# Kernel tuning notes

Hardware: AMD Instinct MI355X
Metric: run time of the kernel (lower is better)

The kernel has to match this reference:

```python
import jax, jax.numpy as jnp
import numpy as np

B, L, D_IN, D_OUT, H = 2, 2048, 1024, 1024, 16
HD = D_OUT // H


def setup_inputs() -> dict:
    key = jax.random.key(0)
    ks = jax.random.split(key, 7)
    s_in = 1.0 / np.sqrt(D_IN)
    s_out = 1.0 / np.sqrt(D_OUT)
    return {
        "x": jax.random.normal(ks[0], (B, L, D_IN), dtype=jnp.float32),
        "Wq": jax.random.uniform(ks[1], (D_OUT, D_IN), jnp.float32, -s_in, s_in),
        "Wg": jax.random.uniform(ks[2], (D_OUT, D_IN), jnp.float32, -s_in, s_in),
        "Wk": jax.random.uniform(ks[3], (D_OUT, D_IN), jnp.float32, -s_in, s_in),
        "Wv": jax.random.uniform(ks[4], (D_OUT, D_IN), jnp.float32, -s_in, s_in),
        "Wo": jax.random.uniform(ks[5], (D_OUT, D_OUT), jnp.float32, -s_out, s_out),
        "bo": jax.random.uniform(ks[6], (D_OUT,), jnp.float32, -s_out, s_out),
    }


def reference(x, Wq, Wg, Wk, Wv, Wo, bo):
    b, l, _ = x.shape
    # projections (torch Linear: x @ W^T)
    q = jnp.einsum('bld,od->blo', x, Wq).reshape(b, l, H, HD)
    g = jnp.einsum('bld,od->blo', x, Wg)
    k = jnp.einsum('bld,od->blo', x, Wk).reshape(b, l, H, HD)
    v = jnp.einsum('bld,od->blo', x, Wv).reshape(b, l, H, HD)
    # attention scores [B,H,L,L]
    scores = jnp.einsum('bqhd,bkhd->bhqk', q, k)
    causal = jnp.tril(jnp.ones((l, l), dtype=bool))
    neg = jnp.finfo(scores.dtype).min
    scores = jnp.where(causal[None, None], scores, neg)
    attn = jax.nn.softmax(scores / np.sqrt(HD), axis=-1)
    ctx = jnp.einsum('bhqk,bkhd->bqhd', attn, v).reshape(b, l, D_OUT)
    ctx = ctx * jax.nn.sigmoid(g)
    return jnp.einsum('blo,po->blp', ctx, Wo) + bo
```

## Files before the change

kernel.cpp:

```cpp
#include <hip/hip_runtime.h>
#include <hip/hip_bf16.h>


typedef __bf16 v8bf __attribute__((ext_vector_type(8)));
typedef __bf16 v4bf __attribute__((ext_vector_type(4)));
typedef float  v4f  __attribute__((ext_vector_type(4)));

using gas_void = const __attribute__((address_space(1))) void*;
using las_void = __attribute__((address_space(3))) void*;

__device__ __forceinline__ void async_ld16(const void* g, void* l) {
  __builtin_amdgcn_global_load_lds((gas_void)g, (las_void)l, 16, 0, 0);
}
__device__ __forceinline__ float fexp2(float x) { return __builtin_amdgcn_exp2f(x); }

#define QSCALE 0.18033688011112042f
#define LOG2E  1.4426950408889634f
#define FIXMAX 8.0f

__global__ void cvt_all_kernel(const float* __restrict__ x,  const float* __restrict__ Wq,
                               const float* __restrict__ Wg, const float* __restrict__ Wk,
                               const float* __restrict__ Wv, const float* __restrict__ Wo,
                               __bf16* __restrict__ xb, __bf16* __restrict__ w3,
                               __bf16* __restrict__ wvb, __bf16* __restrict__ wob) {
  int i = blockIdx.x * 256 + threadIdx.x;
  const float* s; v4bf* d; int j; float sc = 1.f;
  if (i < 1048576)      { s = x;  d = (v4bf*)xb;           j = i; }
  else if (i < 1310720) { s = Wq; d = (v4bf*)w3;           j = i - 1048576; sc = QSCALE; }
  else if (i < 1572864) { s = Wg; d = (v4bf*)w3 + 262144;  j = i - 1310720; }
  else if (i < 1835008) { s = Wk; d = (v4bf*)w3 + 524288;  j = i - 1572864; }
  else if (i < 2097152) { s = Wv; d = (v4bf*)wvb;          j = i - 1835008; }
  else                  { s = Wo; d = (v4bf*)wob;          j = i - 2097152; }
  float4 v = reinterpret_cast<const float4*>(s)[j];
  v4bf o;
  o[0] = (__bf16)(v.x * sc); o[1] = (__bf16)(v.y * sc);
  o[2] = (__bf16)(v.z * sc); o[3] = (__bf16)(v.w * sc);
  d[j] = o;
}

template<bool OUTF32, int BN>
__device__ __forceinline__ void gemm_tile(
    const __bf16* __restrict__ A, const __bf16* __restrict__ B,
    void* __restrict__ C, const float* __restrict__ bias,
    int K, int lda, int ldb, int ldc, int m0, int n0,
    __bf16* As, __bf16* Bs) {
  constexpr int NI = BN / 32;
  const int tid  = threadIdx.x;
  const int w    = tid >> 6;
  const int lane = tid & 63;
  const int fr   = lane & 15;
  const int fq   = lane >> 4;
  const int srow = lane >> 2;
  const int scol = lane & 3;
  const int wr = (w >> 1) * 64, wc = (w & 1) * (BN / 2);

  v4f acc[4][NI];
#pragma unroll
  for (int i = 0; i < 4; ++i)
#pragma unroll
    for (int j = 0; j < NI; ++j)
#pragma unroll
      for (int r = 0; r < 4; ++r) acc[i][j][r] = 0.f;

  for (int k0 = 0; k0 < K; k0 += 32) {
#pragma unroll
    for (int i = 0; i < 2; ++i) {
      const int c = w + i * 4;
      async_ld16(A + (size_t)(m0 + c * 16 + srow) * lda + k0 + scol * 8, (void*)(As + c * 512));
    }
#pragma unroll
    for (int i = 0; i < BN / 64; ++i) {
      const int c = w + i * 4;
      async_ld16(B + (size_t)(n0 + c * 16 + srow) * ldb + k0 + scol * 8, (void*)(Bs + c * 512));
    }
    __syncthreads();

    v8bf a[4], b[NI];
#pragma unroll
    for (int mi = 0; mi < 4; ++mi)
      a[mi] = *reinterpret_cast<const v8bf*>(As + (wr + mi * 16 + fr) * 32 + fq * 8);
#pragma unroll
    for (int ni = 0; ni < NI; ++ni)
      b[ni] = *reinterpret_cast<const v8bf*>(Bs + (wc + ni * 16 + fr) * 32 + fq * 8);
#pragma unroll
    for (int mi = 0; mi < 4; ++mi)
#pragma unroll
      for (int ni = 0; ni < NI; ++ni)
        acc[mi][ni] = __builtin_amdgcn_mfma_f32_16x16x32_bf16(a[mi], b[ni], acc[mi][ni], 0, 0, 0);
    __syncthreads();
  }

#pragma unroll
  for (int mi = 0; mi < 4; ++mi)
#pragma unroll
    for (int ni = 0; ni < NI; ++ni)
#pragma unroll
      for (int r = 0; r < 4; ++r) {
        const int row = m0 + wr + mi * 16 + fq * 4 + r;
        const int col = n0 + wc + ni * 16 + fr;
        const float v = acc[mi][ni][r];
        if (OUTF32) {
          reinterpret_cast<float*>(C)[(size_t)row * ldc + col] = v + bias[col];
        } else {
          reinterpret_cast<__bf16*>(C)[(size_t)row * ldc + col] = (__bf16)v;
        }
      }
}

__global__ __launch_bounds__(256) void proj_kernel(
    const __bf16* __restrict__ xb, const __bf16* __restrict__ w3,
    const __bf16* __restrict__ wvb, __bf16* __restrict__ qgk, __bf16* __restrict__ vt) {
  __shared__ __bf16 As[128 * 32];
  __shared__ __bf16 Bs[128 * 32];
  const int bid = blockIdx.x;
  if (bid < 768) {
    gemm_tile<false, 128>(xb, w3, (void*)qgk, nullptr, 1024, 1024, 1024, 3072,
                          (bid / 24) * 128, (bid % 24) * 128, As, Bs);
  } else {
    const int t = bid - 768;
    gemm_tile<false, 128>(wvb, xb, (void*)vt, nullptr, 1024, 1024, 1024, 4096,
                          (t >> 5) * 128, (t & 31) * 128, As, Bs);
  }
}

template<bool OUTF32, int BN>
__global__ __launch_bounds__(256) void gemm_bt_kernel(
    const __bf16* __restrict__ A, const __bf16* __restrict__ B,
    void* __restrict__ C, const float* __restrict__ bias,
    int K, int lda, int ldb, int ldc) {
  __shared__ __bf16 As[128 * 32];
  __shared__ __bf16 Bs[BN * 32];
  gemm_tile<OUTF32, BN>(A, B, C, bias, K, lda, ldb, ldc,
                        blockIdx.y * 128, blockIdx.x * BN, As, Bs);
}

__global__ __launch_bounds__(256, 4) void attn_kernel(
    const __bf16* __restrict__ QGK, const __bf16* __restrict__ VT,
    __bf16* __restrict__ CTX) {
  constexpr int LD = 3072, L = 2048;
  __shared__ __align__(16) char lds[37888];
  const int w = threadIdx.x >> 6, lane = threadIdx.x & 63;
  const int fr = lane & 15, fq = lane >> 4;
  const int tl = w >> 1, hf = w & 1;
  const int u = blockIdx.x >> 8, v = blockIdx.x & 255;
  const int k = v >> 5;
  const int g = (u == 0) ? k : (u == 1) ? 15 - k : (u == 2) ? 16 + k : 31 - k;
  const int bh = v & 31;
  const int b = bh >> 4, h = bh & 15, hb = h * 64;
  const int qt = 2 * g + tl, q0 = qt * 32, nkt = g + 1;
  const __bf16* base  = QGK + (size_t)b * L * LD;
  const __bf16* vbase = VT + (size_t)hb * 4096 + (size_t)b * L;
  __bf16* pw = (__bf16*)(lds + 16384 + w * 2560);

  v8bf onev;
#pragma unroll
  for (int i = 0; i < 8; ++i) onev[i] = (__bf16)1.0f;

  v8bf qf[2][2];
#pragma unroll
  for (int mi = 0; mi < 2; ++mi)
#pragma unroll
    for (int ks = 0; ks < 2; ++ks)
      qf[mi][ks] = *reinterpret_cast<const v8bf*>(
          base + (size_t)(q0 + mi * 16 + fr) * LD + hb + ks * 32 + fq * 8);

  v4f cacc[2][4], csum[2];
#pragma unroll
  for (int mi = 0; mi < 2; ++mi) {
#pragma unroll
    for (int r = 0; r < 4; ++r) csum[mi][r] = 0.f;
#pragma unroll
    for (int nf = 0; nf < 4; ++nf)
#pragma unroll
      for (int r = 0; r < 4; ++r) cacc[mi][nf][r] = 0.f;
  }

  auto stage = [&](int bi, int k0s) {
    char* bf_ = (char*)lds + bi * 8192;
#pragma unroll
    for (int i = 0; i < 2; ++i) {
      const int slot = i * 256 + w * 64 + lane;
      const int r = slot >> 3;
      const int cc = ((slot & 7) ^ (r & 7)) * 8;
      async_ld16(base + (size_t)(k0s + r) * LD + 2048 + hb + cc,
                 bf_ + (i * 256 + w * 64) * 16);
    }
  };

  stage(0, 0);
  for (int kt = 0; kt < nkt; ++kt) {
    const int k0 = kt * 64;
    const bool last = (kt == nkt - 1);
    v8bf vf[4];
#pragma unroll
    for (int nf = 0; nf < 4; ++nf)
      vf[nf] = *reinterpret_cast<const v8bf*>(
          vbase + (size_t)(nf * 16 + fr) * 4096 + k0 + hf * 32 + fq * 8);
    if (!last) {
      stage((kt + 1) & 1, k0 + 64);
      asm volatile("s_waitcnt vmcnt(6)" ::: "memory");
    } else {
      asm volatile("s_waitcnt vmcnt(4)" ::: "memory");
    }
    __builtin_amdgcn_s_barrier();
    __builtin_amdgcn_sched_barrier(0);

    if (!(last && tl == 0 && hf == 1)) {
      const __bf16* Kt = (const __bf16*)(lds + (kt & 1) * 8192);
      v8bf kf[2][2];
#pragma unroll
      for (int ks = 0; ks < 2; ++ks)
#pragma unroll
        for (int nj = 0; nj < 2; ++nj)
          kf[ks][nj] = *reinterpret_cast<const v8bf*>(
              Kt + (hf * 32 + nj * 16 + fr) * 64 + (((ks * 4 + fq) ^ (fr & 7)) * 8));

      v4f s[2][2];
#pragma unroll
      for (int mi = 0; mi < 2; ++mi)
#pragma unroll
        for (int nj = 0; nj < 2; ++nj)
#pragma unroll
          for (int r = 0; r < 4; ++r) s[mi][nj][r] = 0.f;
      __builtin_amdgcn_s_setprio(1);
#pragma unroll
      for (int ks = 0; ks < 2; ++ks)
#pragma unroll
        for (int mi = 0; mi < 2; ++mi)
#pragma unroll
          for (int nj = 0; nj < 2; ++nj)
            s[mi][nj] = __builtin_amdgcn_mfma_f32_16x16x32_bf16(
                kf[ks][nj], qf[mi][ks], s[mi][nj], 0, 0, 0);
      __builtin_amdgcn_s_setprio(0);

      const bool mask = last && (hf == tl);
#pragma unroll
      for (int mi = 0; mi < 2; ++mi) {
        const int qrow = q0 + mi * 16 + fr;
#pragma unroll
        for (int nj = 0; nj < 2; ++nj) {
          const int kvb = k0 + hf * 32 + nj * 16 + fq * 4;
          v4bf pk;
#pragma unroll
          for (int r = 0; r < 4; ++r) {
            float sv = s[mi][nj][r];
            if (mask && (kvb + r > qrow)) sv = -__builtin_inff();
            pk[r] = (__bf16)fexp2(sv - FIXMAX);
          }
          *reinterpret_cast<v4bf*>(pw + (mi * 16 + fr) * 40 + nj * 16 + fq * 4) = pk;
        }
      }

      v8bf pa[2];
#pragma unroll
      for (int mi = 0; mi < 2; ++mi)
        pa[mi] = *reinterpret_cast<const v8bf*>(pw + (mi * 16 + fr) * 40 + fq * 8);
      __builtin_amdgcn_s_setprio(1);
#pragma unroll
      for (int mi = 0; mi < 2; ++mi)
        csum[mi] = __builtin_amdgcn_mfma_f32_16x16x32_bf16(pa[mi], onev, csum[mi], 0, 0, 0);
#pragma unroll
      for (int nf = 0; nf < 4; ++nf)
#pragma unroll
        for (int mi = 0; mi < 2; ++mi)
          cacc[mi][nf] = __builtin_amdgcn_mfma_f32_16x16x32_bf16(pa[mi], vf[nf], cacc[mi][nf], 0, 0, 0);
      __builtin_amdgcn_s_setprio(0);
    }
    __builtin_amdgcn_sched_barrier(0);
    __builtin_amdgcn_s_barrier();
  }

  __syncthreads();
  float* comb = (float*)(lds + 16384);
  float* slot = comb + (tl * 64 + lane) * 41;
  if (hf == 1) {
#pragma unroll
    for (int mi = 0; mi < 2; ++mi) {
#pragma unroll
      for (int nf = 0; nf < 4; ++nf)
#pragma unroll
        for (int r = 0; r < 4; ++r) slot[mi * 16 + nf * 4 + r] = cacc[mi][nf][r];
#pragma unroll
      for (int r = 0; r < 4; ++r) slot[32 + mi * 4 + r] = csum[mi][r];
    }
  }
  __syncthreads();
  if (hf == 0) {
#pragma unroll
    for (int mi = 0; mi < 2; ++mi) {
#pragma unroll
      for (int nf = 0; nf < 4; ++nf)
#pragma unroll
        for (int r = 0; r < 4; ++r) cacc[mi][nf][r] += slot[mi * 16 + nf * 4 + r];
#pragma unroll
      for (int r = 0; r < 4; ++r) csum[mi][r] += slot[32 + mi * 4 + r];
    }
#pragma unroll
    for (int mi = 0; mi < 2; ++mi)
#pragma unroll
      for (int r = 0; r < 4; ++r) {
        const int grow = q0 + mi * 16 + fq * 4 + r;
        const float rl = 1.f / csum[mi][r];
#pragma unroll
        for (int nf = 0; nf < 4; ++nf) {
          const int col = hb + nf * 16 + fr;
          float vv = cacc[mi][nf][r] * rl;
          const float gt = (float)base[(size_t)grow * LD + 1024 + col];
          vv *= 1.f / (1.f + fexp2(-gt * LOG2E));
          CTX[((size_t)b * L + grow) * 1024 + col] = (__bf16)vv;
        }
      }
  }
}

extern "C" void kernel_launch(void* const* d_in, const int* in_sizes, int n_in,
                              void* d_out, int out_size, void* d_ws, size_t ws_size,
                              hipStream_t stream) {
  const float* x  = (const float*)d_in[0];
  const float* Wq = (const float*)d_in[1];
  const float* Wg = (const float*)d_in[2];
  const float* Wk = (const float*)d_in[3];
  const float* Wv = (const float*)d_in[4];
  const float* Wo = (const float*)d_in[5];
  const float* bo = (const float*)d_in[6];

  char* ws = (char*)d_ws;
  __bf16* xb  = (__bf16*)(ws);
  __bf16* w3  = (__bf16*)(ws + (8u  << 20));
  __bf16* wvb = (__bf16*)(ws + (14u << 20));
  __bf16* wob = (__bf16*)(ws + (16u << 20));
  __bf16* qgk = (__bf16*)(ws + (18u << 20));
  __bf16* vt  = (__bf16*)(ws + (42u << 20));
  __bf16* ctx = (__bf16*)(ws + (50u << 20));

  cvt_all_kernel<<<dim3(9216), dim3(256), 0, stream>>>(x, Wq, Wg, Wk, Wv, Wo,
                                                       xb, w3, wvb, wob);

  proj_kernel<<<dim3(1024), dim3(256), 0, stream>>>(xb, w3, wvb, qgk, vt);

  attn_kernel<<<dim3(1024), dim3(256), 0, stream>>>(qgk, vt, ctx);

  gemm_bt_kernel<true, 64><<<dim3(16, 32), dim3(256), 0, stream>>>(
      ctx, wob, d_out, bo, 1024, 1024, 1024, 1024);
}
```

Baseline: 135.2 us.

## Double-buffer GEMM LDS tiles, swizzle projection blocks, simplify attention sync

The shared GEMM tile routine now uses two LDS buffers. It prefetches the next K-slice with async global-to-LDS loads while running MFMAs on the current one, and raises wave priority around the MFMA block. The projection kernel remaps block indices so that adjacent blocks are spread across the tile grid, aiming for better cache locality. The attention kernel drops its hand-tuned vmcnt waits and raw barriers in favour of one __syncthreads per iteration, which is simpler but may wait on more outstanding loads than needed. LDS use per GEMM block doubles, which could lower occupancy.

```diff
diff --git a/kernel.cpp b/kernel.cpp
--- a/kernel.cpp
+++ b/kernel.cpp
@@ -62,31 +62,43 @@
 #pragma unroll
       for (int r = 0; r < 4; ++r) acc[i][j][r] = 0.f;
 
-  for (int k0 = 0; k0 < K; k0 += 32) {
+  auto stage = [&](int bi, int k0) {
 #pragma unroll
     for (int i = 0; i < 2; ++i) {
       const int c = w + i * 4;
-      async_ld16(A + (size_t)(m0 + c * 16 + srow) * lda + k0 + scol * 8, (void*)(As + c * 512));
+      async_ld16(A + (size_t)(m0 + c * 16 + srow) * lda + k0 + scol * 8,
+                 (void*)(As + bi * 4096 + c * 512));
     }
 #pragma unroll
     for (int i = 0; i < BN / 64; ++i) {
       const int c = w + i * 4;
-      async_ld16(B + (size_t)(n0 + c * 16 + srow) * ldb + k0 + scol * 8, (void*)(Bs + c * 512));
-    }
-    __syncthreads();
-
+      async_ld16(B + (size_t)(n0 + c * 16 + srow) * ldb + k0 + scol * 8,
+                 (void*)(Bs + bi * (BN * 32) + c * 512));
+    }
+  };
+
+  const int nk = K >> 5;
+  stage(0, 0);
+  __syncthreads();
+  for (int t = 0; t < nk; ++t) {
+    if (t + 1 < nk) stage((t + 1) & 1, (t + 1) * 32);
+
+    const __bf16* Ac = As + (t & 1) * 4096;
+    const __bf16* Bc = Bs + (t & 1) * (BN * 32);
     v8bf a[4], b[NI];
 #pragma unroll
     for (int mi = 0; mi < 4; ++mi)
-      a[mi] = *reinterpret_cast<const v8bf*>(As + (wr + mi * 16 + fr) * 32 + fq * 8);
+      a[mi] = *reinterpret_cast<const v8bf*>(Ac + (wr + mi * 16 + fr) * 32 + fq * 8);
 #pragma unroll
     for (int ni = 0; ni < NI; ++ni)
-      b[ni] = *reinterpret_cast<const v8bf*>(Bs + (wc + ni * 16 + fr) * 32 + fq * 8);
+      b[ni] = *reinterpret_cast<const v8bf*>(Bc + (wc + ni * 16 + fr) * 32 + fq * 8);
+    __builtin_amdgcn_s_setprio(1);
 #pragma unroll
     for (int mi = 0; mi < 4; ++mi)
 #pragma unroll
       for (int ni = 0; ni < NI; ++ni)
         acc[mi][ni] = __builtin_amdgcn_mfma_f32_16x16x32_bf16(a[mi], b[ni], acc[mi][ni], 0, 0, 0);
+    __builtin_amdgcn_s_setprio(0);
     __syncthreads();
   }
 
@@ -110,9 +122,9 @@
 __global__ __launch_bounds__(256) void proj_kernel(
     const __bf16* __restrict__ xb, const __bf16* __restrict__ w3,
     const __bf16* __restrict__ wvb, __bf16* __restrict__ qgk, __bf16* __restrict__ vt) {
-  __shared__ __bf16 As[128 * 32];
-  __shared__ __bf16 Bs[128 * 32];
-  const int bid = blockIdx.x;
+  __shared__ __bf16 As[2 * 128 * 32];
+  __shared__ __bf16 Bs[2 * 128 * 32];
+  const int bid = (blockIdx.x & 7) * 128 + (blockIdx.x >> 3);
   if (bid < 768) {
     gemm_tile<false, 128>(xb, w3, (void*)qgk, nullptr, 1024, 1024, 1024, 3072,
                           (bid / 24) * 128, (bid % 24) * 128, As, Bs);
@@ -128,8 +140,8 @@
     const __bf16* __restrict__ A, const __bf16* __restrict__ B,
     void* __restrict__ C, const float* __restrict__ bias,
     int K, int lda, int ldb, int ldc) {
-  __shared__ __bf16 As[128 * 32];
-  __shared__ __bf16 Bs[BN * 32];
+  __shared__ __bf16 As[2 * 128 * 32];
+  __shared__ __bf16 Bs[2 * BN * 32];
   gemm_tile<OUTF32, BN>(A, B, C, bias, K, lda, ldb, ldc,
                         blockIdx.y * 128, blockIdx.x * BN, As, Bs);
 }
@@ -188,6 +200,7 @@
   };
 
   stage(0, 0);
+  __syncthreads();
   for (int kt = 0; kt < nkt; ++kt) {
     const int k0 = kt * 64;
     const bool last = (kt == nkt - 1);
@@ -196,14 +209,7 @@
     for (int nf = 0; nf < 4; ++nf)
       vf[nf] = *reinterpret_cast<const v8bf*>(
           vbase + (size_t)(nf * 16 + fr) * 4096 + k0 + hf * 32 + fq * 8);
-    if (!last) {
-      stage((kt + 1) & 1, k0 + 64);
-      asm volatile("s_waitcnt vmcnt(6)" ::: "memory");
-    } else {
-      asm volatile("s_waitcnt vmcnt(4)" ::: "memory");
-    }
-    __builtin_amdgcn_s_barrier();
-    __builtin_amdgcn_sched_barrier(0);
+    if (!last) stage((kt + 1) & 1, k0 + 64);
 
     if (!(last && tl == 0 && hf == 1)) {
       const __bf16* Kt = (const __bf16*)(lds + (kt & 1) * 8192);
@@ -266,11 +272,9 @@
           cacc[mi][nf] = __builtin_amdgcn_mfma_f32_16x16x32_bf16(pa[mi], vf[nf], cacc[mi][nf], 0, 0, 0);
       __builtin_amdgcn_s_setprio(0);
     }
-    __builtin_amdgcn_sched_barrier(0);
-    __builtin_amdgcn_s_barrier();
-  }
-
-  __syncthreads();
+    __syncthreads();
+  }
+
   float* comb = (float*)(lds + 16384);
   float* slot = comb + (tl * 64 + lane) * 41;
   if (hf == 1) {
```

New measurement: 133.6 us. Within noise of the previous version (-1.2%).
